# Optimization experiments

Hardware: AMD Instinct MI355X
Metric: run time of the kernel (lower is better)

Reference implementation:

```python
import jax, jax.numpy as jnp
import numpy as np

BLOCK_SIZE = 4
CHANNEL_USE = 7
SAMPS = 20  # samps_per_symb in the original forward
LEAK = 0.01  # nn.LeakyReLU default slope


def _make_filters(K=101):
    # Deterministic stand-ins for h_lowpass.txt / h_pulseshape.txt
    n = np.arange(K) - (K - 1) / 2
    fc = 1.0 / SAMPS
    h_lp = (np.sinc(2 * fc * n) * np.hamming(K) * 2 * fc).astype(np.float32)
    h_ps = (np.sinc(n / SAMPS) * np.hamming(K)).astype(np.float32)
    return h_lp, h_ps


def _conv_same(sig, h):
    # Batched equivalent of np.convolve(row, h, 'same') for odd-length h.
    # sig: [N, L] float, h: [K] float. True convolution => flip kernel for lax correlation.
    K = h.shape[0]
    pad = (K - 1) // 2
    out = jax.lax.conv_general_dilated(
        sig[:, None, :], h[::-1][None, None, :],
        window_strides=(1,), padding=[(pad, pad)],
        dimension_numbers=('NCH', 'OIH', 'NCH'))
    return out[:, 0, :]


def setup_inputs() -> dict:
    key = jax.random.key(0)
    B, IN, CD = 131072, 16, 7
    ks = jax.random.split(key, 6)

    def lin(k, fi, fo):
        bound = 1.0 / np.sqrt(fi)
        kw, kb = jax.random.split(k)
        W = jax.random.uniform(kw, (fo, fi), jnp.float32, -bound, bound)
        b = jax.random.uniform(kb, (fo,), jnp.float32, -bound, bound)
        return W, b

    We1, be1 = lin(ks[0], IN, IN)
    We2, be2 = lin(ks[1], IN, CD)
    Wd1, bd1 = lin(ks[2], CD, IN)
    Wd2, bd2 = lin(ks[3], IN, IN)
    x = jax.random.normal(ks[4], (B, IN), jnp.float32)
    noise = jax.random.normal(ks[5], (B, CD), jnp.float32)
    h_lp, h_ps = _make_filters()
    return dict(x=x, We1=We1, be1=be1, We2=We2, be2=be2,
                Wd1=Wd1, bd1=bd1, Wd2=Wd2, bd2=bd2,
                h_lowpass=jnp.asarray(h_lp), h_pulseshape=jnp.asarray(h_ps),
                noise=noise, snr=4)


def reference(x, We1, be1, We2, be2, Wd1, bd1, Wd2, bd2,
              h_lowpass, h_pulseshape, noise, snr):
    B = x.shape[0]
    # ---- encoder MLP + global-norm scaling to power 70 ----
    h = jnp.dot(x, We1.T) + be1
    h = jnp.where(h >= 0, h, LEAK * h)
    enc = jnp.dot(h, We2.T) + be2
    enc = enc / jnp.linalg.norm(enc) * 70.0

    CD = enc.shape[1]          # bits_per_code
    M = 2 ** CD                # PSK order

    # ---- non-differentiable PSK channel (torch does .cpu().detach()) ----
    e = jax.lax.stop_gradient(enc)
    xi = jnp.round(e).astype(jnp.int32)           # int(np.round(.)) per element
    sign = jnp.where(xi < 0, -1.0, 1.0)           # sign_mask
    idx = jnp.mod(jnp.abs(xi), M)                  # bin() drops sign; values < M in practice
    phase = (2.0 * jnp.pi / M) * idx.astype(jnp.float32)
    sr, si = jnp.cos(phase), jnp.sin(phase)        # commpy PSK constellation exp(2*pi*i/M)

    def up(s):  # zero-stuff upsample by SAMPS: [B, CD] -> [B, CD*SAMPS]
        u = jnp.zeros((B, CD, SAMPS), s.dtype).at[:, :, 0].set(s)
        return u.reshape(B, CD * SAMPS)

    sig = jnp.concatenate([up(sr), up(si)], axis=0)  # real/imag stacked: [2B, L]
    sig = _conv_same(sig, h_pulseshape)
    sig = _conv_same(sig, h_lowpass)
    sig = _conv_same(sig, h_pulseshape)
    y = sig[:, ::SAMPS] * SAMPS                      # downsample, [2B, CD]
    yr, yi = y[:B], y[B:]
    # hard PSK demod = nearest unit-circle point = phase quantization
    ang = jnp.arctan2(yi, yr)
    idx_hat = jnp.mod(jnp.round(ang * (M / (2.0 * jnp.pi))), M)
    res = idx_hat.astype(jnp.float32) * sign

    # ---- AWGN ----
    rate = BLOCK_SIZE / CHANNEL_USE
    snr_lin = 10.0 ** (0.1 * snr)
    res = res + noise / jnp.sqrt(jnp.float32(2.0 * rate * snr_lin))

    # ---- decoder MLP ----
    d = jnp.dot(res, Wd1.T) + bd1
    d = jnp.where(d >= 0, d, LEAK * d)
    out = jnp.dot(d, Wd2.T) + bd2
    return out
```

## Files before the change

kernel.cpp:

```cpp
#include <hip/hip_runtime.h>
#include <math.h>

#define IN_DIM   16
#define CD       7
#define SAMPS    20
#define KFILT    101
#define SIGLEN   140
#define MCONST   128


__global__ __launch_bounds__(256) void k1_enc(
    const float* __restrict__ x,
    const float* __restrict__ We1, const float* __restrict__ be1,
    const float* __restrict__ We2, const float* __restrict__ be2,
    const float* __restrict__ h_lp, const float* __restrict__ h_ps,
    float* __restrict__ enc, double* __restrict__ partials,
    float* __restrict__ Gd, int B)
{
    int t   = threadIdx.x;
    int bid = blockIdx.x;
    int row = bid * 256 + t;

    __shared__ float  sW1[256], sW2[112], sb1[16], sb2[7];
    __shared__ double wred[4];
    __shared__ float  curp[240], nxtp[240];
    __shared__ float  hA[KFILT], hB[KFILT];

    sW1[t] = We1[t];
    if (t < 112) sW2[t] = We2[t];
    if (t < 16)  sb1[t] = be1[t];
    if (t < 7)   sb2[t] = be2[t];
    if (bid < CD && t < KFILT) { hA[t] = h_ps[t]; hB[t] = h_lp[t]; }
    __syncthreads();

    double ss = 0.0;
    if (row < B) {
        const float4* xp = reinterpret_cast<const float4*>(x + (size_t)row * IN_DIM);
        float4 v0 = xp[0], v1 = xp[1], v2 = xp[2], v3 = xp[3];
        float xr[16] = {v0.x,v0.y,v0.z,v0.w, v1.x,v1.y,v1.z,v1.w,
                        v2.x,v2.y,v2.z,v2.w, v3.x,v3.y,v3.z,v3.w};
        float h[16];
        #pragma unroll
        for (int i = 0; i < 16; ++i) {
            float acc = sb1[i];
            #pragma unroll
            for (int j = 0; j < 16; ++j) acc = fmaf(sW1[i*16+j], xr[j], acc);
            h[i] = (acc >= 0.f) ? acc : 0.01f * acc;
        }
        float e[8];
        #pragma unroll
        for (int o = 0; o < CD; ++o) {
            float acc = sb2[o];
            #pragma unroll
            for (int i = 0; i < 16; ++i) acc = fmaf(sW2[o*16+i], h[i], acc);
            e[o] = acc;
            ss += (double)acc * (double)acc;
        }
        e[7] = 0.f;
        float4* ep = reinterpret_cast<float4*>(enc + (size_t)row * 8);
        ep[0] = make_float4(e[0], e[1], e[2], e[3]);
        ep[1] = make_float4(e[4], e[5], e[6], e[7]);
    }
    double v = ss;
    #pragma unroll
    for (int off = 32; off > 0; off >>= 1) v += __shfl_down(v, off);
    if ((t & 63) == 0) wred[t >> 6] = v;
    __syncthreads();
    if (t == 0) partials[bid] = (wred[0] + wred[1]) + (wred[2] + wred[3]);

    if (bid < CD) {
        if (t < 240) { curp[t] = 0.0f; nxtp[t] = 0.0f; }
        __syncthreads();
        if (t < SIGLEN) {
            int m = t + 50 - SAMPS * bid;
            curp[t + 50] = (m >= 0 && m < KFILT) ? hA[m] : 0.0f;
        }
        __syncthreads();
        for (int f = 0; f < 2; ++f) {
            const float* h = (f == 0) ? hB : hA;
            if (t < SIGLEN) {
                float a0 = 0.f, a1 = 0.f;
                for (int m = 0; m <= 50; ++m)   a0 = fmaf(h[m], curp[t + 100 - m], a0);
                for (int m = 51; m < KFILT; ++m) a1 = fmaf(h[m], curp[t + 100 - m], a1);
                nxtp[t + 50] = a0 + a1;
            }
            __syncthreads();
            if (t < SIGLEN) curp[t + 50] = nxtp[t + 50];
            __syncthreads();
        }
        if (t < CD) Gd[t * CD + bid] = (float)SAMPS * curp[t * SAMPS + 50];
    }
}

__global__ __launch_bounds__(256) void k2_main(
    const float* __restrict__ enc,
    const float* __restrict__ Wd1, const float* __restrict__ bd1,
    const float* __restrict__ Wd2, const float* __restrict__ bd2,
    const float* __restrict__ noise, const int* __restrict__ snr_p,
    const double* __restrict__ partials, const float* __restrict__ Gd,
    float* __restrict__ out, int B, int NBP)
{
    int t   = threadIdx.x;
    int bid = blockIdx.x;
    int base_row = bid * 512;

    __shared__ float  sV1[112], sc1[16], sV2[256], sc2[16];
    __shared__ float  str[2 * MCONST];
    __shared__ float  sG[49];
    __shared__ double wred[4];
    __shared__ float  snz[512 * CD];
    __shared__ float  sinv, ninv;

    sV2[t] = Wd2[t];
    if (t < 112) sV1[t] = Wd1[t];
    if (t < 16)  { sc1[t] = bd1[t]; sc2[t] = bd2[t]; }
    if (t < 49)  sG[t] = Gd[t];
    if (t < MCONST) {
        float ph = (float)(2.0 * 3.14159265358979323846 / (double)MCONST) * (float)t;
        str[t]          = cosf(ph);
        str[MCONST + t] = sinf(ph);
    }
    {
        size_t nb  = (size_t)base_row * CD;
        size_t lim = (size_t)B * CD;
        for (int i = t; i < 512 * CD; i += 256)
            if (nb + i < lim) snz[i] = noise[nb + i];
    }
    {
        double s = 0.0;
        for (int i = t; i < NBP; i += 256) s += partials[i];
        #pragma unroll
        for (int off = 32; off > 0; off >>= 1) s += __shfl_down(s, off);
        if ((t & 63) == 0) wred[t >> 6] = s;
    }
    __syncthreads();
    if (t == 0)
        sinv = 70.0f / (float)sqrt((wred[0] + wred[1]) + (wred[2] + wred[3]));
    if (t == 1) {
        int iv = *snr_p;
        float sv = (iv >= -1000 && iv <= 1000) ? (float)iv
                                               : *reinterpret_cast<const float*>(snr_p);
        float snr_lin = powf(10.0f, 0.1f * sv);
        ninv = 1.0f / sqrtf((float)(8.0 / 7.0) * snr_lin);
    }
    __syncthreads();

    #pragma unroll
    for (int c = 0; c < 2; ++c) {
        int lrow = c * 256 + t;
        int row  = base_row + lrow;
        if (row >= B) continue;

        const float4* ep = reinterpret_cast<const float4*>(enc + (size_t)row * 8);
        float4 e0 = ep[0], e1 = ep[1];
        float ev[7] = {e0.x, e0.y, e0.z, e0.w, e1.x, e1.y, e1.z};

        float sr[CD], si[CD], sgn[CD];
        #pragma unroll
        for (int o = 0; o < CD; ++o) {
            float es = ev[o] * sinv;
            float rv = rintf(es);
            int xi = (int)rv;
            sgn[o] = (xi < 0) ? -1.0f : 1.0f;
            int idx = (xi < 0 ? -xi : xi) & (MCONST - 1);
            sr[o] = str[idx];
            si[o] = str[MCONST + idx];
        }

        float res[CD];
        #pragma unroll
        for (int k = 0; k < CD; ++k) {
            float yr = 0.f, yi = 0.f;
            #pragma unroll
            for (int cc = 0; cc < CD; ++cc) {
                float g = sG[k * CD + cc];
                yr = fmaf(g, sr[cc], yr);
                yi = fmaf(g, si[cc], yi);
            }
            float ang = atan2f(yi, yr);
            float q = ang * (float)(128.0 / (2.0 * 3.14159265358979323846));
            float r = rintf(q);
            float m = (r < 0.0f) ? r + 128.0f : r;
            res[k] = fmaf(snz[lrow * CD + k], ninv, m * sgn[k]);
        }

        float dd[16];
        #pragma unroll
        for (int i = 0; i < 16; ++i) {
            float acc = sc1[i];
            #pragma unroll
            for (int cc = 0; cc < CD; ++cc) acc = fmaf(sV1[i*CD+cc], res[cc], acc);
            dd[i] = (acc >= 0.f) ? acc : 0.01f * acc;
        }
        float4* op = reinterpret_cast<float4*>(out + (size_t)row * IN_DIM);
        #pragma unroll
        for (int q4 = 0; q4 < 4; ++q4) {
            float o0[4];
            #pragma unroll
            for (int u = 0; u < 4; ++u) {
                int i = q4 * 4 + u;
                float acc = sc2[i];
                #pragma unroll
                for (int j = 0; j < 16; ++j) acc = fmaf(sV2[i*16+j], dd[j], acc);
                o0[u] = acc;
            }
            op[q4] = make_float4(o0[0], o0[1], o0[2], o0[3]);
        }
    }
}

extern "C" void kernel_launch(void* const* d_in, const int* in_sizes, int n_in,
                              void* d_out, int out_size, void* d_ws, size_t ws_size,
                              hipStream_t stream)
{
    const float* x    = (const float*)d_in[0];
    const float* We1  = (const float*)d_in[1];
    const float* be1  = (const float*)d_in[2];
    const float* We2  = (const float*)d_in[3];
    const float* be2  = (const float*)d_in[4];
    const float* Wd1  = (const float*)d_in[5];
    const float* bd1  = (const float*)d_in[6];
    const float* Wd2  = (const float*)d_in[7];
    const float* bd2  = (const float*)d_in[8];
    const float* h_lp = (const float*)d_in[9];
    const float* h_ps = (const float*)d_in[10];
    const float* noise= (const float*)d_in[11];
    const int*   snr  = (const int*)d_in[12];
    float* out = (float*)d_out;

    int B   = in_sizes[0] / IN_DIM;
    int NB  = (B + 255) / 256;
    int NB2 = (B + 511) / 512;

    char* ws = (char*)d_ws;
    double* partials = (double*)(ws + 0);
    float*  Gd       = (float*) (ws + 4096);
    float*  enc      = (float*) (ws + 8192);

    k1_enc<<<NB, 256, 0, stream>>>(x, We1, be1, We2, be2, h_lp, h_ps,
                                   enc, partials, Gd, B);
    k2_main<<<NB2, 256, 0, stream>>>(enc, Wd1, bd1, Wd2, bd2, noise, snr,
                                     partials, Gd, out, B, NB);
}
```

Baseline: 29.23 us.

## Fuse encoder and decoder kernels with an in-kernel grid-wide norm reduction

```diff
diff --git a/kernel.cpp b/kernel.cpp
--- a/kernel.cpp
+++ b/kernel.cpp
@@ -8,6 +8,250 @@
 #define SIGLEN   140
 #define MCONST   128
 
+
+__device__ __forceinline__ unsigned ld_u32(const void* p) {
+    return __hip_atomic_load((const unsigned*)p, __ATOMIC_RELAXED,
+                             __HIP_MEMORY_SCOPE_AGENT);
+}
+__device__ __forceinline__ void st_u32(void* p, unsigned v) {
+    __hip_atomic_store((unsigned*)p, v, __ATOMIC_RELAXED,
+                       __HIP_MEMORY_SCOPE_AGENT);
+}
+__device__ __forceinline__ unsigned add_u32(void* p) {
+    return __hip_atomic_fetch_add((unsigned*)p, 1u, __ATOMIC_RELAXED,
+                                  __HIP_MEMORY_SCOPE_AGENT);
+}
+__device__ __forceinline__ double ld_f64(const void* p) {
+    return __hip_atomic_load((const double*)p, __ATOMIC_RELAXED,
+                             __HIP_MEMORY_SCOPE_AGENT);
+}
+__device__ __forceinline__ void st_f64(void* p, double v) {
+    __hip_atomic_store((double*)p, v, __ATOMIC_RELAXED,
+                       __HIP_MEMORY_SCOPE_AGENT);
+}
+__device__ __forceinline__ float ld_f32(const void* p) {
+    return __hip_atomic_load((const float*)p, __ATOMIC_RELAXED,
+                             __HIP_MEMORY_SCOPE_AGENT);
+}
+__device__ __forceinline__ void st_f32(void* p, float v) {
+    __hip_atomic_store((float*)p, v, __ATOMIC_RELAXED,
+                       __HIP_MEMORY_SCOPE_AGENT);
+}
+
+__global__ __launch_bounds__(256, 2) void k_fused(
+    const float* __restrict__ x,
+    const float* __restrict__ We1, const float* __restrict__ be1,
+    const float* __restrict__ We2, const float* __restrict__ be2,
+    const float* __restrict__ Wd1, const float* __restrict__ bd1,
+    const float* __restrict__ Wd2, const float* __restrict__ bd2,
+    const float* __restrict__ h_lp, const float* __restrict__ h_ps,
+    const float* __restrict__ noise, const int* __restrict__ snr_p,
+    char* __restrict__ ws, float* __restrict__ out, int B, int NB)
+{
+    int t   = threadIdx.x;
+    int bid = blockIdx.x;
+    int row = bid * 256 + t;
+
+    double* partials = (double*)(ws + 0);
+    float*  GR       = (float*) (ws + 4096);
+    char*   L0       = ws + 8192;
+    char*   GS       = ws + 10240;
+    char*   ROOT     = ws + 12288;
+    char*   FLAG     = ws + 12544;
+
+    __shared__ float    sW1[256], sW2[112], sb1[16], sb2[7];
+    __shared__ float    sV1[112], sV2[256], sc1[16], sc2[16];
+    __shared__ float    str[2 * MCONST];
+    __shared__ float    snz[256 * CD];
+    __shared__ double   wred[4];
+    __shared__ float    sG[49];
+    __shared__ float    curp[240], nxtp[240];
+    __shared__ float    hA[KFILT], hB[KFILT];
+    __shared__ unsigned sNormBits;
+    __shared__ float    ninv;
+
+    sW1[t] = We1[t];  sV2[t] = Wd2[t];
+    if (t < 112) { sW2[t] = We2[t]; sV1[t] = Wd1[t]; }
+    if (t < 16)  { sb1[t] = be1[t]; sc1[t] = bd1[t]; sc2[t] = bd2[t]; }
+    if (t < 7)   sb2[t] = be2[t];
+    if (bid < CD && t < KFILT) { hA[t] = h_ps[t]; hB[t] = h_lp[t]; }
+    if (t < MCONST) {
+        float ph = (float)(2.0 * 3.14159265358979323846 / (double)MCONST) * (float)t;
+        str[t]          = cosf(ph);
+        str[MCONST + t] = sinf(ph);
+    }
+    __syncthreads();
+
+    float e[CD];
+    double ss = 0.0;
+    if (row < B) {
+        const float4* xp = reinterpret_cast<const float4*>(x + (size_t)row * IN_DIM);
+        float4 v0 = xp[0], v1 = xp[1], v2 = xp[2], v3 = xp[3];
+        float xr[16] = {v0.x,v0.y,v0.z,v0.w, v1.x,v1.y,v1.z,v1.w,
+                        v2.x,v2.y,v2.z,v2.w, v3.x,v3.y,v3.z,v3.w};
+        float h[16];
+        #pragma unroll
+        for (int i = 0; i < 16; ++i) {
+            float acc = sb1[i];
+            #pragma unroll
+            for (int j = 0; j < 16; ++j) acc = fmaf(sW1[i*16+j], xr[j], acc);
+            h[i] = (acc >= 0.f) ? acc : 0.01f * acc;
+        }
+        #pragma unroll
+        for (int o = 0; o < CD; ++o) {
+            float acc = sb2[o];
+            #pragma unroll
+            for (int i = 0; i < 16; ++i) acc = fmaf(sW2[o*16+i], h[i], acc);
+            e[o] = acc;
+            ss += (double)acc * (double)acc;
+        }
+    }
+    double v = ss;
+    #pragma unroll
+    for (int off = 32; off > 0; off >>= 1) v += __shfl_down(v, off);
+    if ((t & 63) == 0) wred[t >> 6] = v;
+    __syncthreads();
+    if (t == 0) st_f64(&partials[bid], (wred[0] + wred[1]) + (wred[2] + wred[3]));
+
+    if (bid < CD) {
+        if (t < 240) { curp[t] = 0.0f; nxtp[t] = 0.0f; }
+        __syncthreads();
+        if (t < SIGLEN) {
+            int m = t + 50 - SAMPS * bid;
+            curp[t + 50] = (m >= 0 && m < KFILT) ? hA[m] : 0.0f;
+        }
+        __syncthreads();
+        for (int f = 0; f < 2; ++f) {
+            const float* h = (f == 0) ? hB : hA;
+            if (t < SIGLEN) {
+                float a0 = 0.f, a1 = 0.f;
+                for (int m = 0; m <= 50; ++m)    a0 = fmaf(h[m], curp[t + 100 - m], a0);
+                for (int m = 51; m < KFILT; ++m) a1 = fmaf(h[m], curp[t + 100 - m], a1);
+                nxtp[t + 50] = a0 + a1;
+            }
+            __syncthreads();
+            if (t < SIGLEN) curp[t + 50] = nxtp[t + 50];
+            __syncthreads();
+        }
+        if (t < CD) {
+            float gv = (float)SAMPS * curp[t * SAMPS + 50];
+            #pragma unroll
+            for (int r = 0; r < 8; ++r)
+                st_f32(&GR[r * 64 + t * CD + bid], gv);
+        }
+    }
+
+    {
+        size_t nb  = (size_t)bid * (256 * CD);
+        size_t lim = (size_t)B * CD;
+        for (int i = t; i < 256 * CD; i += 256)
+            if (nb + i < lim) snz[i] = noise[nb + i];
+    }
+    if (t == 1) {
+        int iv = *snr_p;
+        float sv = (iv >= -1000 && iv <= 1000) ? (float)iv
+                                               : *reinterpret_cast<const float*>(snr_p);
+        float snr_lin = powf(10.0f, 0.1f * sv);
+        ninv = 1.0f / sqrtf((float)(8.0 / 7.0) * snr_lin);
+    }
+
+    __syncthreads();
+    if (t < 64) {
+        asm volatile("s_waitcnt vmcnt(0)" ::: "memory");
+        int g       = bid >> 6;
+        int gbase   = g << 6;
+        int gsize   = (NB - gbase < 64) ? (NB - gbase) : 64;
+        int ngroups = (NB + 63) >> 6;
+
+        unsigned aret = 0;
+        if (t == 0) aret = add_u32(L0 + (size_t)g * 256);
+        aret = __shfl(aret, 0);
+        if ((int)aret == gsize - 1) {
+            double p = (t < gsize) ? ld_f64(&partials[gbase + t]) : 0.0;
+            #pragma unroll
+            for (int off = 32; off > 0; off >>= 1) p += __shfl_down(p, off);
+            unsigned rret = 0;
+            if (t == 0) {
+                st_f64(GS + (size_t)g * 256, p);
+                asm volatile("s_waitcnt vmcnt(0)" ::: "memory");
+                rret = add_u32(ROOT);
+            }
+            rret = __shfl(rret, 0);
+            if ((int)rret == ngroups - 1) {
+                double gsv = (t < ngroups) ? ld_f64(GS + (size_t)t * 256) : 0.0;
+                #pragma unroll
+                for (int off = 32; off > 0; off >>= 1) gsv += __shfl_down(gsv, off);
+                unsigned bits = 0;
+                if (t == 0) bits = __float_as_uint((float)sqrt(gsv));
+                bits = __shfl(bits, 0);
+                if (t < 8) st_u32(FLAG + (size_t)t * 256, bits);
+            }
+        }
+        if (t == 0) {
+            unsigned b2;
+            while ((b2 = ld_u32(FLAG + (size_t)(bid & 7) * 256)) == 0u)
+                __builtin_amdgcn_s_sleep(4);
+            sNormBits = b2;
+        }
+        if (t < 49) sG[t] = ld_f32(&GR[(size_t)(bid & 7) * 64 + t]);
+    }
+    __syncthreads();
+    float sinv = 70.0f / __uint_as_float(sNormBits);
+
+    if (row >= B) return;
+
+    float sr[CD], si[CD], sgn[CD];
+    #pragma unroll
+    for (int o = 0; o < CD; ++o) {
+        float es = e[o] * sinv;
+        float rv = rintf(es);
+        int xi = (int)rv;
+        sgn[o] = (xi < 0) ? -1.0f : 1.0f;
+        int idx = (xi < 0 ? -xi : xi) & (MCONST - 1);
+        sr[o] = str[idx];
+        si[o] = str[MCONST + idx];
+    }
+
+    float res[CD];
+    #pragma unroll
+    for (int k = 0; k < CD; ++k) {
+        float yr = 0.f, yi = 0.f;
+        #pragma unroll
+        for (int cc = 0; cc < CD; ++cc) {
+            float g = sG[k * CD + cc];
+            yr = fmaf(g, sr[cc], yr);
+            yi = fmaf(g, si[cc], yi);
+        }
+        float ang = atan2f(yi, yr);
+        float q = ang * (float)(128.0 / (2.0 * 3.14159265358979323846));
+        float r = rintf(q);
+        float m = (r < 0.0f) ? r + 128.0f : r;
+        res[k] = fmaf(snz[t * CD + k], ninv, m * sgn[k]);
+    }
+
+    float dd[16];
+    #pragma unroll
+    for (int i = 0; i < 16; ++i) {
+        float acc = sc1[i];
+        #pragma unroll
+        for (int cc = 0; cc < CD; ++cc) acc = fmaf(sV1[i*CD+cc], res[cc], acc);
+        dd[i] = (acc >= 0.f) ? acc : 0.01f * acc;
+    }
+    float4* op = reinterpret_cast<float4*>(out + (size_t)row * IN_DIM);
+    #pragma unroll
+    for (int q4 = 0; q4 < 4; ++q4) {
+        float o0[4];
+        #pragma unroll
+        for (int u = 0; u < 4; ++u) {
+            int i = q4 * 4 + u;
+            float acc = sc2[i];
+            #pragma unroll
+            for (int j = 0; j < 16; ++j) acc = fmaf(sV2[i*16+j], dd[j], acc);
+            o0[u] = acc;
+        }
+        op[q4] = make_float4(o0[0], o0[1], o0[2], o0[3]);
+    }
+}
 
 __global__ __launch_bounds__(256) void k1_enc(
     const float* __restrict__ x,
@@ -17,22 +261,17 @@
     float* __restrict__ enc, double* __restrict__ partials,
     float* __restrict__ Gd, int B)
 {
-    int t   = threadIdx.x;
-    int bid = blockIdx.x;
-    int row = bid * 256 + t;
-
+    int t = threadIdx.x, bid = blockIdx.x, row = bid * 256 + t;
     __shared__ float  sW1[256], sW2[112], sb1[16], sb2[7];
     __shared__ double wred[4];
     __shared__ float  curp[240], nxtp[240];
     __shared__ float  hA[KFILT], hB[KFILT];
-
     sW1[t] = We1[t];
     if (t < 112) sW2[t] = We2[t];
     if (t < 16)  sb1[t] = be1[t];
     if (t < 7)   sb2[t] = be2[t];
     if (bid < CD && t < KFILT) { hA[t] = h_ps[t]; hB[t] = h_lp[t]; }
     __syncthreads();
-
     double ss = 0.0;
     if (row < B) {
         const float4* xp = reinterpret_cast<const float4*>(x + (size_t)row * IN_DIM);
@@ -53,8 +292,7 @@
             float acc = sb2[o];
             #pragma unroll
             for (int i = 0; i < 16; ++i) acc = fmaf(sW2[o*16+i], h[i], acc);
-            e[o] = acc;
-            ss += (double)acc * (double)acc;
+            e[o] = acc; ss += (double)acc * (double)acc;
         }
         e[7] = 0.f;
         float4* ep = reinterpret_cast<float4*>(enc + (size_t)row * 8);
@@ -67,7 +305,6 @@
     if ((t & 63) == 0) wred[t >> 6] = v;
     __syncthreads();
     if (t == 0) partials[bid] = (wred[0] + wred[1]) + (wred[2] + wred[3]);
-
     if (bid < CD) {
         if (t < 240) { curp[t] = 0.0f; nxtp[t] = 0.0f; }
         __syncthreads();
@@ -80,7 +317,7 @@
             const float* h = (f == 0) ? hB : hA;
             if (t < SIGLEN) {
                 float a0 = 0.f, a1 = 0.f;
-                for (int m = 0; m <= 50; ++m)   a0 = fmaf(h[m], curp[t + 100 - m], a0);
+                for (int m = 0; m <= 50; ++m)    a0 = fmaf(h[m], curp[t + 100 - m], a0);
                 for (int m = 51; m < KFILT; ++m) a1 = fmaf(h[m], curp[t + 100 - m], a1);
                 nxtp[t + 50] = a0 + a1;
             }
@@ -100,29 +337,23 @@
     const double* __restrict__ partials, const float* __restrict__ Gd,
     float* __restrict__ out, int B, int NBP)
 {
-    int t   = threadIdx.x;
-    int bid = blockIdx.x;
-    int base_row = bid * 512;
-
+    int t = threadIdx.x, bid = blockIdx.x, base_row = bid * 512;
     __shared__ float  sV1[112], sc1[16], sV2[256], sc2[16];
     __shared__ float  str[2 * MCONST];
     __shared__ float  sG[49];
     __shared__ double wred[4];
     __shared__ float  snz[512 * CD];
     __shared__ float  sinv, ninv;
-
     sV2[t] = Wd2[t];
     if (t < 112) sV1[t] = Wd1[t];
     if (t < 16)  { sc1[t] = bd1[t]; sc2[t] = bd2[t]; }
     if (t < 49)  sG[t] = Gd[t];
     if (t < MCONST) {
         float ph = (float)(2.0 * 3.14159265358979323846 / (double)MCONST) * (float)t;
-        str[t]          = cosf(ph);
-        str[MCONST + t] = sinf(ph);
+        str[t] = cosf(ph); str[MCONST + t] = sinf(ph);
     }
     {
-        size_t nb  = (size_t)base_row * CD;
-        size_t lim = (size_t)B * CD;
+        size_t nb = (size_t)base_row * CD, lim = (size_t)B * CD;
         for (int i = t; i < 512 * CD; i += 256)
             if (nb + i < lim) snz[i] = noise[nb + i];
     }
@@ -134,8 +365,7 @@
         if ((t & 63) == 0) wred[t >> 6] = s;
     }
     __syncthreads();
-    if (t == 0)
-        sinv = 70.0f / (float)sqrt((wred[0] + wred[1]) + (wred[2] + wred[3]));
+    if (t == 0) sinv = 70.0f / (float)sqrt((wred[0] + wred[1]) + (wred[2] + wred[3]));
     if (t == 1) {
         int iv = *snr_p;
         float sv = (iv >= -1000 && iv <= 1000) ? (float)iv
@@ -144,17 +374,13 @@
         ninv = 1.0f / sqrtf((float)(8.0 / 7.0) * snr_lin);
     }
     __syncthreads();
-
     #pragma unroll
     for (int c = 0; c < 2; ++c) {
-        int lrow = c * 256 + t;
-        int row  = base_row + lrow;
+        int lrow = c * 256 + t, row = base_row + lrow;
         if (row >= B) continue;
-
         const float4* ep = reinterpret_cast<const float4*>(enc + (size_t)row * 8);
         float4 e0 = ep[0], e1 = ep[1];
         float ev[7] = {e0.x, e0.y, e0.z, e0.w, e1.x, e1.y, e1.z};
-
         float sr[CD], si[CD], sgn[CD];
         #pragma unroll
         for (int o = 0; o < CD; ++o) {
@@ -163,10 +389,8 @@
             int xi = (int)rv;
             sgn[o] = (xi < 0) ? -1.0f : 1.0f;
             int idx = (xi < 0 ? -xi : xi) & (MCONST - 1);
-            sr[o] = str[idx];
-            si[o] = str[MCONST + idx];
-        }
-
+            sr[o] = str[idx]; si[o] = str[MCONST + idx];
+        }
         float res[CD];
         #pragma unroll
         for (int k = 0; k < CD; ++k) {
@@ -174,8 +398,7 @@
             #pragma unroll
             for (int cc = 0; cc < CD; ++cc) {
                 float g = sG[k * CD + cc];
-                yr = fmaf(g, sr[cc], yr);
-                yi = fmaf(g, si[cc], yi);
+                yr = fmaf(g, sr[cc], yr); yi = fmaf(g, si[cc], yi);
             }
             float ang = atan2f(yi, yr);
             float q = ang * (float)(128.0 / (2.0 * 3.14159265358979323846));
@@ -183,7 +406,6 @@
             float m = (r < 0.0f) ? r + 128.0f : r;
             res[k] = fmaf(snz[lrow * CD + k], ninv, m * sgn[k]);
         }
-
         float dd[16];
         #pragma unroll
         for (int i = 0; i < 16; ++i) {
@@ -228,17 +450,24 @@
     const int*   snr  = (const int*)d_in[12];
     float* out = (float*)d_out;
 
-    int B   = in_sizes[0] / IN_DIM;
-    int NB  = (B + 255) / 256;
-    int NB2 = (B + 511) / 512;
+    int B  = in_sizes[0] / IN_DIM;
+    int NB = (B + 255) / 256;
 
     char* ws = (char*)d_ws;
-    double* partials = (double*)(ws + 0);
-    float*  Gd       = (float*) (ws + 4096);
-    float*  enc      = (float*) (ws + 8192);
-
-    k1_enc<<<NB, 256, 0, stream>>>(x, We1, be1, We2, be2, h_lp, h_ps,
-                                   enc, partials, Gd, B);
-    k2_main<<<NB2, 256, 0, stream>>>(enc, Wd1, bd1, Wd2, bd2, noise, snr,
-                                     partials, Gd, out, B, NB);
-}
+
+    if (NB <= 512) {
+        hipMemsetAsync(ws + 8192, 0, 6400, stream);
+        k_fused<<<NB, 256, 0, stream>>>(x, We1, be1, We2, be2, Wd1, bd1,
+                                        Wd2, bd2, h_lp, h_ps, noise, snr,
+                                        ws, out, B, NB);
+    } else {
+        double* partials = (double*)(ws + 0);
+        float*  Gd       = (float*) (ws + 4096);
+        float*  enc      = (float*) (ws + 16384);
+        int NB2 = (B + 511) / 512;
+        k1_enc<<<NB, 256, 0, stream>>>(x, We1, be1, We2, be2, h_lp, h_ps,
+                                       enc, partials, Gd, B);
+        k2_main<<<NB2, 256, 0, stream>>>(enc, Wd1, bd1, Wd2, bd2, noise, snr,
+                                         partials, Gd, out, B, NB);
+    }
+}
```

After: 28.95 us. No clear change (-1.0%).
